# Kernel optimization log

Measured on AMD Instinct MI355X. Metric: run time of the kernel, lower is better.

The kernel has to match this reference:

```python
import jax, jax.numpy as jnp
import numpy as np
from jax import lax

C = 64
B, H, W = 4, 192, 192


def conv2d(x, w, b):
    # x: [B,C,H,W], w: [O,I,3,3] (OIHW), stride 1, pad 1
    y = lax.conv_general_dilated(x, w, (1, 1), ((1, 1), (1, 1)),
                                 dimension_numbers=("NCHW", "OIHW", "NCHW"))
    return y + b[None, :, None, None]


def csm(x, w1, b1, w2, b2):
    # residual block: conv3x3 -> relu -> conv3x3 + skip
    return x + conv2d(jax.nn.relu(conv2d(x, w1, b1)), w2, b2)


def setup_inputs() -> dict:
    key = jax.random.key(0)
    ks = jax.random.split(key, 12)
    s = 1.0 / np.sqrt(C * 9)
    def cw(k):
        return jax.random.uniform(k, (C, C, 3, 3), jnp.float32, -s, s)
    def cb(k):
        return jax.random.uniform(k, (C,), jnp.float32, -s, s)
    return {
        "low1": jax.random.normal(ks[0], (B, C, H, W), jnp.float32),
        "low2": jax.random.normal(ks[1], (B, C, H, W), jnp.float32),
        "fe1_w1": cw(ks[2]), "fe1_b1": cb(ks[3]),
        "fe1_w2": cw(ks[4]), "fe1_b2": cb(ks[5]),
        "fe2_w1": cw(ks[6]), "fe2_b1": cb(ks[7]),
        "fe2_w2": cw(ks[8]), "fe2_b2": cb(ks[9]),
        "conv_w": cw(ks[10]), "conv_b": cb(ks[11]),
    }


def reference(low1, low2, fe1_w1, fe1_b1, fe1_w2, fe1_b2,
              fe2_w1, fe2_b1, fe2_w2, fe2_b2, conv_w, conv_b):
    Q1 = conv2d(csm(low1, fe1_w1, fe1_b1, fe1_w2, fe1_b2), conv_w, conv_b)
    K1 = conv2d(csm(low2, fe1_w1, fe1_b1, fe1_w2, fe1_b2), conv_w, conv_b)
    Q2 = conv2d(csm(low1, fe2_w1, fe2_b1, fe2_w2, fe2_b2), conv_w, conv_b)
    K2 = conv2d(csm(low2, fe2_w1, fe2_b1, fe2_w2, fe2_b2), conv_w, conv_b)

    # per-row cross-width scores: [B,H,W,W] (no scaling; softmax then relu)
    score1 = jax.nn.relu(jax.nn.softmax(jnp.einsum("bchw,bchv->bhwv", Q1, K1), axis=-1))
    score2 = jax.nn.relu(jax.nn.softmax(jnp.einsum("bchw,bchv->bhwv", Q2, K2), axis=-1))

    def apply_score(score, feat):
        # out[b,c,h,w] = sum_v score[b,h,w,v] * feat[b,c,h,v]
        return jnp.einsum("bhwv,bchv->bchw", score, feat)

    def apply_score_T(score, feat):
        # out[b,c,h,w] = sum_v score[b,h,v,w] * feat[b,c,h,v]
        return jnp.einsum("bhvw,bchv->bchw", score, feat)

    right2left1 = apply_score(score1, low2)
    right2left2 = apply_score(score2, low2)
    left2right1 = apply_score_T(score1, low1)
    left2right2 = apply_score_T(score2, low1)
    left2right2left = apply_score(score2, left2right1)
    right2left2right = apply_score_T(score2, right2left1)

    left = low1 + right2left1 + right2left2 + left2right2left
    right = low2 + left2right1 + left2right2 + right2left2right
    return (left, right)
```

## Files before the change

kernel.cpp:

```cpp
#include <hip/hip_runtime.h>
#include <stdint.h>

#define NB 4
#define NC 64
#define NH 192
#define NW 192

typedef __attribute__((ext_vector_type(8))) short bf16x8;
typedef __attribute__((ext_vector_type(4))) float f32x4;
typedef unsigned short u16;
typedef unsigned int u32;

__device__ inline float bf2f(u16 x){ u32 u = ((u32)x) << 16; return __builtin_bit_cast(float, u); }
__device__ inline u16 f2bf(float f){ u32 u = __builtin_bit_cast(u32, f); u32 r = u + 0x7fffu + ((u >> 16) & 1u); return (u16)(r >> 16); }
__device__ inline bf16x8 packf8(float4 a, float4 b){
  bf16x8 r;
  r[0]=(short)f2bf(a.x); r[1]=(short)f2bf(a.y); r[2]=(short)f2bf(a.z); r[3]=(short)f2bf(a.w);
  r[4]=(short)f2bf(b.x); r[5]=(short)f2bf(b.y); r[6]=(short)f2bf(b.z); r[7]=(short)f2bf(b.w);
  return r;
}

__global__ void wxform_k(const float* __restrict__ w0, const float* __restrict__ w1,
                         const float* __restrict__ w2, const float* __restrict__ w3,
                         const float* __restrict__ w4, u16* __restrict__ out){
  int idx = blockIdx.x * 256 + threadIdx.x;
  if (idx >= 5 * 36864) return;
  int t = idx / 36864, e = idx % 36864;
  int r = e >> 12, rem = e & 4095, co = rem >> 6, ci = rem & 63;
  const float* src = (t == 0) ? w0 : (t == 1) ? w1 : (t == 2) ? w2 : (t == 3) ? w3 : w4;
  out[idx] = f2bf(src[co * 576 + ci * 9 + r]);
}

__global__ __launch_bounds__(192) void nchw2nhwc_k(const float* __restrict__ in, u16* __restrict__ out){
  int bh = blockIdx.x; int b = bh / NH, h = bh % NH;
  int w = threadIdx.x;
  u16 v[64];
  const float* p = in + ((size_t)b * NC * NH + h) * NW + w;
#pragma unroll
  for (int c = 0; c < 64; ++c) v[c] = f2bf(p[(size_t)c * NH * NW]);
  uint4* q4 = (uint4*)(out + ((size_t)bh * NW + w) * NC);
#pragma unroll
  for (int i = 0; i < 8; ++i){
    uint4 t;
    t.x = (u32)v[i*8+0] | ((u32)v[i*8+1] << 16);
    t.y = (u32)v[i*8+2] | ((u32)v[i*8+3] << 16);
    t.z = (u32)v[i*8+4] | ((u32)v[i*8+5] << 16);
    t.w = (u32)v[i*8+6] | ((u32)v[i*8+7] << 16);
    q4[i] = t;
  }
}

__global__ __launch_bounds__(256) void bf2f_k(const u16* __restrict__ in, float* __restrict__ out){
  int i = blockIdx.x * 256 + threadIdx.x;
  uint4 v = ((const uint4*)in)[i];
  float4 f0, f1;
  f0.x = bf2f((u16)(v.x & 0xffff)); f0.y = bf2f((u16)(v.x >> 16));
  f0.z = bf2f((u16)(v.y & 0xffff)); f0.w = bf2f((u16)(v.y >> 16));
  f1.x = bf2f((u16)(v.z & 0xffff)); f1.y = bf2f((u16)(v.z >> 16));
  f1.z = bf2f((u16)(v.w & 0xffff)); f1.w = bf2f((u16)(v.w >> 16));
  ((float4*)out)[2*i]   = f0;
  ((float4*)out)[2*i+1] = f1;
}

__global__ __launch_bounds__(256) void conv3_k(const u16* __restrict__ in, const u16* __restrict__ wt,
    const float* __restrict__ bias, const u16* __restrict__ skip, u16* __restrict__ out, int relu){
  __shared__ __align__(16) u16 xr[3][98 * 72];
  int blk = blockIdx.x;
  int wh = blk & 1;
  int strip = blk >> 1;
  int g0 = strip * 3;
  int b = g0 / NH, h0 = g0 % NH;
  int wstart = wh * 96;
  int tid = threadIdx.x;
  int wvv = tid >> 6, lane = tid & 63, l15 = lane & 15, qd = lane >> 4;
  int mh = wvv >> 1, wq = wvv & 1;

#define STAGE(hh_) do { \
    int hh = (hh_); \
    int slot = ((hh % 3) + 3) % 3; \
    bool rowok = (hh >= 0) && (hh < NH); \
    const u16* src = in + (((size_t)b * NH + (rowok ? hh : 0)) * NW) * 64; \
    for (int k2 = tid; k2 < 784; k2 += 256){ \
      int x = k2 >> 3, part = k2 & 7; \
      int w = wstart - 1 + x; \
      uint4 val = make_uint4(0,0,0,0); \
      if (rowok && w >= 0 && w < NW) val = *(const uint4*)(src + (size_t)w * 64 + part * 8); \
      *(uint4*)&xr[slot][x * 72 + part * 8] = val; \
    } \
  } while(0)

  STAGE(h0 - 1);
  STAGE(h0);
  for (int j = 0; j < 3; ++j){
    int h = h0 + j;
    STAGE(h + 1);
    __syncthreads();
    f32x4 acc[2][3];
#pragma unroll
    for (int mt = 0; mt < 2; ++mt)
#pragma unroll
      for (int nt = 0; nt < 3; ++nt) acc[mt][nt] = (f32x4){0.f,0.f,0.f,0.f};
#pragma unroll
    for (int r = 0; r < 9; ++r){
      int ky = r / 3, kx = r % 3;
      int hs = h - 1 + ky;
      const u16* xbase = xr[((hs % 3) + 3) % 3];
#pragma unroll
      for (int ks = 0; ks < 2; ++ks){
        int ci = ks * 32 + qd * 8;
        const u16* wp = wt + r * 4096 + ci;
        bf16x8 a0 = *(const bf16x8*)(wp + (mh * 32 + l15) * 64);
        bf16x8 a1 = *(const bf16x8*)(wp + (mh * 32 + 16 + l15) * 64);
#pragma unroll
        for (int nt = 0; nt < 3; ++nt){
          int x = wq * 48 + nt * 16 + l15 + kx;
          bf16x8 bfr = *(const bf16x8*)&xr[0][0 + ((hs % 3) + 3) % 3 * 0];
          bfr = *(const bf16x8*)&xbase[x * 72 + ci];
          acc[0][nt] = __builtin_amdgcn_mfma_f32_16x16x32_bf16(a0, bfr, acc[0][nt], 0, 0, 0);
          acc[1][nt] = __builtin_amdgcn_mfma_f32_16x16x32_bf16(a1, bfr, acc[1][nt], 0, 0, 0);
        }
      }
    }
    size_t rowbase = ((size_t)(b * NH + h)) * NW * 64;
#pragma unroll
    for (int mt = 0; mt < 2; ++mt){
      int co0 = mh * 32 + mt * 16 + qd * 4;
      float4 bb = *(const float4*)(bias + co0);
#pragma unroll
      for (int nt = 0; nt < 3; ++nt){
        int w = wstart + wq * 48 + nt * 16 + l15;
        size_t o = rowbase + (size_t)w * 64 + co0;
        float v0 = acc[mt][nt][0] + bb.x, v1 = acc[mt][nt][1] + bb.y;
        float v2 = acc[mt][nt][2] + bb.z, v3 = acc[mt][nt][3] + bb.w;
        if (relu){ v0 = fmaxf(v0,0.f); v1 = fmaxf(v1,0.f); v2 = fmaxf(v2,0.f); v3 = fmaxf(v3,0.f); }
        if (skip){
          uint2 ss = *(const uint2*)(skip + o);
          v0 += bf2f((u16)(ss.x & 0xffff)); v1 += bf2f((u16)(ss.x >> 16));
          v2 += bf2f((u16)(ss.y & 0xffff)); v3 += bf2f((u16)(ss.y >> 16));
        }
        uint2 st;
        st.x = (u32)f2bf(v0) | ((u32)f2bf(v1) << 16);
        st.y = (u32)f2bf(v2) | ((u32)f2bf(v3) << 16);
        *(uint2*)(out + o) = st;
      }
    }
    __syncthreads();
  }
#undef STAGE
}

template<int XYF32>
__global__ __launch_bounds__(256) void attn_k(const u16* __restrict__ Q, const u16* __restrict__ K,
    const void* __restrict__ Xv, const void* __restrict__ Yv,
    u16* __restrict__ outA, u16* __restrict__ outB){
  __shared__ __align__(16) u16 P [192 * 200];
  __shared__ __align__(16) u16 Pt[192 * 200];
  int bh = blockIdx.x, b = bh / NH, h = bh % NH;
  int tid = threadIdx.x, wv = tid >> 6, lane = tid & 63, l15 = lane & 15, qd = lane >> 4;
  size_t rowo = (size_t)bh * NW * 64;
  const u16* Qr = Q + rowo; const u16* Kr = K + rowo;
  const size_t CS = (size_t)NH * NW;
  size_t xb0 = (size_t)b * 64 * CS + (size_t)h * NW;
  const float* Xf = (const float*)Xv; const float* Yf = (const float*)Yv;
  const u16* Xb = (const u16*)Xv; const u16* Yb = (const u16*)Yv;

#pragma unroll 1
  for (int mi = 0; mi < 3; ++mi){
    int mt = wv * 3 + mi;
    f32x4 s[12];
#pragma unroll
    for (int nt = 0; nt < 12; ++nt) s[nt] = (f32x4){0,0,0,0};
#pragma unroll
    for (int ks = 0; ks < 2; ++ks){
      bf16x8 aq = *(const bf16x8*)(Qr + (mt * 16 + l15) * 64 + ks * 32 + qd * 8);
#pragma unroll
      for (int nt = 0; nt < 12; ++nt){
        bf16x8 bk = *(const bf16x8*)(Kr + (nt * 16 + l15) * 64 + ks * 32 + qd * 8);
        s[nt] = __builtin_amdgcn_mfma_f32_16x16x32_bf16(aq, bk, s[nt], 0, 0, 0);
      }
    }
#pragma unroll
    for (int rg = 0; rg < 4; ++rg){
      float mx = -1e30f;
#pragma unroll
      for (int nt = 0; nt < 12; ++nt) mx = fmaxf(mx, s[nt][rg]);
      mx = fmaxf(mx, __shfl_xor(mx, 1));
      mx = fmaxf(mx, __shfl_xor(mx, 2));
      mx = fmaxf(mx, __shfl_xor(mx, 4));
      mx = fmaxf(mx, __shfl_xor(mx, 8));
      float sum = 0.f;
#pragma unroll
      for (int nt = 0; nt < 12; ++nt){ float ev = __expf(s[nt][rg] - mx); s[nt][rg] = ev; sum += ev; }
      sum += __shfl_xor(sum, 1);
      sum += __shfl_xor(sum, 2);
      sum += __shfl_xor(sum, 4);
      sum += __shfl_xor(sum, 8);
      float inv = 1.f / sum;
      int w = mt * 16 + qd * 4 + rg;
#pragma unroll
      for (int nt = 0; nt < 12; ++nt){
        float val = s[nt][rg] * inv;
        s[nt][rg] = val;
        P[w * 200 + nt * 16 + l15] = f2bf(val);
      }
    }
#pragma unroll
    for (int nt = 0; nt < 12; ++nt){
      uint2 pk;
      pk.x = (u32)f2bf(s[nt][0]) | ((u32)f2bf(s[nt][1]) << 16);
      pk.y = (u32)f2bf(s[nt][2]) | ((u32)f2bf(s[nt][3]) << 16);
      *(uint2*)&Pt[(nt * 16 + l15) * 200 + mt * 16 + qd * 4] = pk;
    }
  }
  __syncthreads();

  f32x4 accA[3][4], accB[3][4];
#pragma unroll
  for (int ni = 0; ni < 3; ++ni)
#pragma unroll
    for (int mt = 0; mt < 4; ++mt){ accA[ni][mt] = (f32x4){0,0,0,0}; accB[ni][mt] = (f32x4){0,0,0,0}; }
#pragma unroll 1
  for (int ks = 0; ks < 6; ++ks){
    int v0 = ks * 32 + qd * 8;
    bf16x8 aX[4], aY[4];
#pragma unroll
    for (int mt = 0; mt < 4; ++mt){
      int c = mt * 16 + l15;
      size_t off = xb0 + (size_t)c * CS + v0;
      if (XYF32){
        float4 x0 = *(const float4*)(Xf + off), x1 = *(const float4*)(Xf + off + 4);
        float4 y0 = *(const float4*)(Yf + off), y1 = *(const float4*)(Yf + off + 4);
        aX[mt] = packf8(x0, x1); aY[mt] = packf8(y0, y1);
      } else {
        aX[mt] = *(const bf16x8*)(Xb + off);
        aY[mt] = *(const bf16x8*)(Yb + off);
      }
    }
#pragma unroll
    for (int ni = 0; ni < 3; ++ni){
      int wrow = (wv * 3 + ni) * 16 + l15;
      bf16x8 bP  = *(const bf16x8*)&P [wrow * 200 + v0];
      bf16x8 bPt = *(const bf16x8*)&Pt[wrow * 200 + v0];
#pragma unroll
      for (int mt = 0; mt < 4; ++mt){
        accA[ni][mt] = __builtin_amdgcn_mfma_f32_16x16x32_bf16(aX[mt], bP,  accA[ni][mt], 0, 0, 0);
        accB[ni][mt] = __builtin_amdgcn_mfma_f32_16x16x32_bf16(aY[mt], bPt, accB[ni][mt], 0, 0, 0);
      }
    }
  }
#pragma unroll
  for (int ni = 0; ni < 3; ++ni){
    int w = (wv * 3 + ni) * 16 + l15;
#pragma unroll
    for (int mt = 0; mt < 4; ++mt){
#pragma unroll
      for (int rg = 0; rg < 4; ++rg){
        int c = mt * 16 + qd * 4 + rg;
        size_t o = xb0 + (size_t)c * CS + w;
        float ra = XYF32 ? Yf[o] : bf2f(Yb[o]);
        float rb = XYF32 ? Xf[o] : bf2f(Xb[o]);
        outA[o] = f2bf(accA[ni][mt][rg] + ra);
        outB[o] = f2bf(accB[ni][mt][rg] + rb);
      }
    }
  }
}

extern "C" void kernel_launch(void* const* d_in, const int* in_sizes, int n_in,
                              void* d_out, int out_size, void* d_ws, size_t ws_size,
                              hipStream_t stream){
  const float* low1 = (const float*)d_in[0];
  const float* low2 = (const float*)d_in[1];
  const float* b11 = (const float*)d_in[3];
  const float* b12 = (const float*)d_in[5];
  const float* b21 = (const float*)d_in[7];
  const float* b22 = (const float*)d_in[9];
  const float* bcv = (const float*)d_in[11];
  const size_t BUF = (size_t)NB * NH * NW * NC;
  u16* WT = (u16*)d_ws;
  u16* s1 = WT + 184320;
  u16* s2 = s1 + BUF;
  u16* o1 = (u16*)d_out;
  u16* o2 = o1 + BUF;
  u16* o3 = o1 + 2 * BUF;
  u16* o4 = o1 + 3 * BUF;
  float* outL = (float*)d_out;
  float* outR = outL + BUF;

  wxform_k<<<dim3(720), dim3(256), 0, stream>>>(
      (const float*)d_in[2], (const float*)d_in[4], (const float*)d_in[6],
      (const float*)d_in[8], (const float*)d_in[10], WT);
  nchw2nhwc_k<<<dim3(NB * NH), dim3(192), 0, stream>>>(low1, o1);
  nchw2nhwc_k<<<dim3(NB * NH), dim3(192), 0, stream>>>(low2, o2);

#define CONV(in_, wti, bias_, skip_, out_, relu_) \
  conv3_k<<<dim3(512), dim3(256), 0, stream>>>(in_, WT + (wti) * 36864, bias_, skip_, out_, relu_)

  CONV(o1, 0, b11, (const u16*)nullptr, o3, 1);
  CONV(o3, 1, b12, o1, o4, 0);
  CONV(o4, 4, bcv, (const u16*)nullptr, s1, 0);
  CONV(o2, 0, b11, (const u16*)nullptr, o3, 1);
  CONV(o3, 1, b12, o2, o4, 0);
  CONV(o4, 4, bcv, (const u16*)nullptr, s2, 0);
  attn_k<1><<<dim3(NB * NH), dim3(256), 0, stream>>>(s1, s2, (const void*)low2, (const void*)low1, o3, o4);
  CONV(o1, 2, b21, (const u16*)nullptr, s1, 1);
  CONV(s1, 3, b22, o1, s2, 0);
  CONV(s2, 4, bcv, (const u16*)nullptr, o1, 0);
  CONV(o2, 2, b21, (const u16*)nullptr, s1, 1);
  CONV(s1, 3, b22, o2, s2, 0);
  CONV(s2, 4, bcv, (const u16*)nullptr, o2, 0);
  attn_k<0><<<dim3(NB * NH), dim3(256), 0, stream>>>(o1, o2, (const void*)o4, (const void*)o3, s1, s2);
  bf2f_k<<<dim3((int)(BUF / 8 / 256)), dim3(256), 0, stream>>>(s1, outL);
  bf2f_k<<<dim3((int)(BUF / 8 / 256)), dim3(256), 0, stream>>>(s2, outR);
#undef CONV
}
```

Measured before the change: 639.3 us.

## Batch paired convs per launch, shrink conv tiles, drop attention transpose buffer

Each conv launch now handles both input streams at once, with 64-wide width chunks, giving 1536 blocks with launch bounds of 4 instead of 512 blocks per tensor; this cuts the number of launches and raises occupancy. The attention kernel drops its separate transposed-probability LDS buffer and runs the two apply passes one after another, building the transposed operand with strided 16-bit gathers from the single buffer. The final attention writes the left output directly in fp32, which removes one bf16-to-fp32 conversion kernel, and buffers are reused so the residual-conv output can be written in place. The risks are less weight reuse in the smaller conv tiles and bank-conflicted scalar LDS gathers in the transposed pass.

```diff
diff --git a/kernel.cpp b/kernel.cpp
--- a/kernel.cpp
+++ b/kernel.cpp
@@ -62,27 +62,32 @@
   ((float4*)out)[2*i+1] = f1;
 }
 
-__global__ __launch_bounds__(256) void conv3_k(const u16* __restrict__ in, const u16* __restrict__ wt,
-    const float* __restrict__ bias, const u16* __restrict__ skip, u16* __restrict__ out, int relu){
-  __shared__ __align__(16) u16 xr[3][98 * 72];
+__global__ __launch_bounds__(256, 4) void conv3_k(
+    const u16* __restrict__ in1, const u16* __restrict__ in2,
+    const u16* __restrict__ wt, const float* __restrict__ bias,
+    const u16* __restrict__ skip1, const u16* __restrict__ skip2,
+    u16* __restrict__ out1, u16* __restrict__ out2, int relu){
+  __shared__ __align__(16) u16 xr[3][66 * 72];
   int blk = blockIdx.x;
-  int wh = blk & 1;
-  int strip = blk >> 1;
-  int g0 = strip * 3;
-  int b = g0 / NH, h0 = g0 % NH;
-  int wstart = wh * 96;
+  int inp = blk & 1, rest = blk >> 1;
+  int chunk = rest % 3, strip = rest / 3;
+  const u16* in = inp ? in2 : in1;
+  const u16* skip = inp ? skip2 : skip1;
+  u16* out = inp ? out2 : out1;
+  int g0 = strip * 3, b = g0 / NH, h0 = g0 % NH;
+  int w0c = chunk * 64;
   int tid = threadIdx.x;
   int wvv = tid >> 6, lane = tid & 63, l15 = lane & 15, qd = lane >> 4;
   int mh = wvv >> 1, wq = wvv & 1;
 
 #define STAGE(hh_) do { \
     int hh = (hh_); \
-    int slot = ((hh % 3) + 3) % 3; \
+    int slot = (hh + 3) % 3; \
     bool rowok = (hh >= 0) && (hh < NH); \
-    const u16* src = in + (((size_t)b * NH + (rowok ? hh : 0)) * NW) * 64; \
-    for (int k2 = tid; k2 < 784; k2 += 256){ \
+    const u16* src = in + ((size_t)(b * NH + (rowok ? hh : 0)) * NW) * 64; \
+    for (int k2 = tid; k2 < 528; k2 += 256){ \
       int x = k2 >> 3, part = k2 & 7; \
-      int w = wstart - 1 + x; \
+      int w = w0c - 1 + x; \
       uint4 val = make_uint4(0,0,0,0); \
       if (rowok && w >= 0 && w < NW) val = *(const uint4*)(src + (size_t)w * 64 + part * 8); \
       *(uint4*)&xr[slot][x * 72 + part * 8] = val; \
@@ -95,16 +100,16 @@
     int h = h0 + j;
     STAGE(h + 1);
     __syncthreads();
-    f32x4 acc[2][3];
+    f32x4 acc[2][2];
 #pragma unroll
     for (int mt = 0; mt < 2; ++mt)
 #pragma unroll
-      for (int nt = 0; nt < 3; ++nt) acc[mt][nt] = (f32x4){0.f,0.f,0.f,0.f};
+      for (int nt = 0; nt < 2; ++nt) acc[mt][nt] = (f32x4){0.f,0.f,0.f,0.f};
 #pragma unroll
     for (int r = 0; r < 9; ++r){
       int ky = r / 3, kx = r % 3;
       int hs = h - 1 + ky;
-      const u16* xbase = xr[((hs % 3) + 3) % 3];
+      const u16* xb = xr[(hs + 3) % 3];
 #pragma unroll
       for (int ks = 0; ks < 2; ++ks){
         int ci = ks * 32 + qd * 8;
@@ -112,10 +117,9 @@
         bf16x8 a0 = *(const bf16x8*)(wp + (mh * 32 + l15) * 64);
         bf16x8 a1 = *(const bf16x8*)(wp + (mh * 32 + 16 + l15) * 64);
 #pragma unroll
-        for (int nt = 0; nt < 3; ++nt){
-          int x = wq * 48 + nt * 16 + l15 + kx;
-          bf16x8 bfr = *(const bf16x8*)&xr[0][0 + ((hs % 3) + 3) % 3 * 0];
-          bfr = *(const bf16x8*)&xbase[x * 72 + ci];
+        for (int nt = 0; nt < 2; ++nt){
+          int x = wq * 32 + nt * 16 + l15 + kx;
+          bf16x8 bfr = *(const bf16x8*)&xb[x * 72 + ci];
           acc[0][nt] = __builtin_amdgcn_mfma_f32_16x16x32_bf16(a0, bfr, acc[0][nt], 0, 0, 0);
           acc[1][nt] = __builtin_amdgcn_mfma_f32_16x16x32_bf16(a1, bfr, acc[1][nt], 0, 0, 0);
         }
@@ -127,8 +131,8 @@
       int co0 = mh * 32 + mt * 16 + qd * 4;
       float4 bb = *(const float4*)(bias + co0);
 #pragma unroll
-      for (int nt = 0; nt < 3; ++nt){
-        int w = wstart + wq * 48 + nt * 16 + l15;
+      for (int nt = 0; nt < 2; ++nt){
+        int w = w0c + wq * 32 + nt * 16 + l15;
         size_t o = rowbase + (size_t)w * 64 + co0;
         float v0 = acc[mt][nt][0] + bb.x, v1 = acc[mt][nt][1] + bb.y;
         float v2 = acc[mt][nt][2] + bb.z, v3 = acc[mt][nt][3] + bb.w;
@@ -149,12 +153,11 @@
 #undef STAGE
 }
 
-template<int XYF32>
-__global__ __launch_bounds__(256) void attn_k(const u16* __restrict__ Q, const u16* __restrict__ K,
+template<int XYF32, int AF32>
+__global__ __launch_bounds__(256, 2) void attn_k(const u16* __restrict__ Q, const u16* __restrict__ K,
     const void* __restrict__ Xv, const void* __restrict__ Yv,
-    u16* __restrict__ outA, u16* __restrict__ outB){
-  __shared__ __align__(16) u16 P [192 * 200];
-  __shared__ __align__(16) u16 Pt[192 * 200];
+    void* __restrict__ outAv, u16* __restrict__ outB){
+  __shared__ __align__(16) u16 P[192 * 200];
   int bh = blockIdx.x, b = bh / NH, h = bh % NH;
   int tid = threadIdx.x, wv = tid >> 6, lane = tid & 63, l15 = lane & 15, qd = lane >> 4;
   size_t rowo = (size_t)bh * NW * 64;
@@ -198,70 +201,97 @@
       float inv = 1.f / sum;
       int w = mt * 16 + qd * 4 + rg;
 #pragma unroll
-      for (int nt = 0; nt < 12; ++nt){
-        float val = s[nt][rg] * inv;
-        s[nt][rg] = val;
-        P[w * 200 + nt * 16 + l15] = f2bf(val);
-      }
-    }
-#pragma unroll
-    for (int nt = 0; nt < 12; ++nt){
-      uint2 pk;
-      pk.x = (u32)f2bf(s[nt][0]) | ((u32)f2bf(s[nt][1]) << 16);
-      pk.y = (u32)f2bf(s[nt][2]) | ((u32)f2bf(s[nt][3]) << 16);
-      *(uint2*)&Pt[(nt * 16 + l15) * 200 + mt * 16 + qd * 4] = pk;
+      for (int nt = 0; nt < 12; ++nt)
+        P[w * 200 + nt * 16 + l15] = f2bf(s[nt][rg] * inv);
     }
   }
   __syncthreads();
 
-  f32x4 accA[3][4], accB[3][4];
-#pragma unroll
-  for (int ni = 0; ni < 3; ++ni)
-#pragma unroll
-    for (int mt = 0; mt < 4; ++mt){ accA[ni][mt] = (f32x4){0,0,0,0}; accB[ni][mt] = (f32x4){0,0,0,0}; }
+  {
+    f32x4 acc[3][4];
+#pragma unroll
+    for (int ni = 0; ni < 3; ++ni)
+#pragma unroll
+      for (int mt = 0; mt < 4; ++mt) acc[ni][mt] = (f32x4){0,0,0,0};
 #pragma unroll 1
-  for (int ks = 0; ks < 6; ++ks){
-    int v0 = ks * 32 + qd * 8;
-    bf16x8 aX[4], aY[4];
-#pragma unroll
-    for (int mt = 0; mt < 4; ++mt){
-      int c = mt * 16 + l15;
-      size_t off = xb0 + (size_t)c * CS + v0;
-      if (XYF32){
-        float4 x0 = *(const float4*)(Xf + off), x1 = *(const float4*)(Xf + off + 4);
-        float4 y0 = *(const float4*)(Yf + off), y1 = *(const float4*)(Yf + off + 4);
-        aX[mt] = packf8(x0, x1); aY[mt] = packf8(y0, y1);
-      } else {
-        aX[mt] = *(const bf16x8*)(Xb + off);
-        aY[mt] = *(const bf16x8*)(Yb + off);
+    for (int ks = 0; ks < 6; ++ks){
+      int v0 = ks * 32 + qd * 8;
+      bf16x8 a[4];
+#pragma unroll
+      for (int mt = 0; mt < 4; ++mt){
+        size_t off = xb0 + (size_t)(mt * 16 + l15) * CS + v0;
+        if (XYF32){
+          float4 x0 = *(const float4*)(Xf + off), x1 = *(const float4*)(Xf + off + 4);
+          a[mt] = packf8(x0, x1);
+        } else a[mt] = *(const bf16x8*)(Xb + off);
+      }
+#pragma unroll
+      for (int ni = 0; ni < 3; ++ni){
+        int wrow = (wv * 3 + ni) * 16 + l15;
+        bf16x8 bP = *(const bf16x8*)&P[wrow * 200 + v0];
+#pragma unroll
+        for (int mt = 0; mt < 4; ++mt)
+          acc[ni][mt] = __builtin_amdgcn_mfma_f32_16x16x32_bf16(a[mt], bP, acc[ni][mt], 0, 0, 0);
       }
     }
 #pragma unroll
     for (int ni = 0; ni < 3; ++ni){
-      int wrow = (wv * 3 + ni) * 16 + l15;
-      bf16x8 bP  = *(const bf16x8*)&P [wrow * 200 + v0];
-      bf16x8 bPt = *(const bf16x8*)&Pt[wrow * 200 + v0];
+      int w = (wv * 3 + ni) * 16 + l15;
+#pragma unroll
+      for (int mt = 0; mt < 4; ++mt)
+#pragma unroll
+        for (int rg = 0; rg < 4; ++rg){
+          int c = mt * 16 + qd * 4 + rg;
+          size_t o = xb0 + (size_t)c * CS + w;
+          float ra = XYF32 ? Yf[o] : bf2f(Yb[o]);
+          float val = acc[ni][mt][rg] + ra;
+          if (AF32) ((float*)outAv)[o] = val;
+          else ((u16*)outAv)[o] = f2bf(val);
+        }
+    }
+  }
+  __syncthreads();
+  {
+    f32x4 acc[3][4];
+#pragma unroll
+    for (int ni = 0; ni < 3; ++ni)
+#pragma unroll
+      for (int mt = 0; mt < 4; ++mt) acc[ni][mt] = (f32x4){0,0,0,0};
+#pragma unroll 1
+    for (int ks = 0; ks < 6; ++ks){
+      int v0 = ks * 32 + qd * 8;
+      bf16x8 a[4];
 #pragma unroll
       for (int mt = 0; mt < 4; ++mt){
-        accA[ni][mt] = __builtin_amdgcn_mfma_f32_16x16x32_bf16(aX[mt], bP,  accA[ni][mt], 0, 0, 0);
-        accB[ni][mt] = __builtin_amdgcn_mfma_f32_16x16x32_bf16(aY[mt], bPt, accB[ni][mt], 0, 0, 0);
-      }
-    }
-  }
-#pragma unroll
-  for (int ni = 0; ni < 3; ++ni){
-    int w = (wv * 3 + ni) * 16 + l15;
-#pragma unroll
-    for (int mt = 0; mt < 4; ++mt){
-#pragma unroll
-      for (int rg = 0; rg < 4; ++rg){
-        int c = mt * 16 + qd * 4 + rg;
-        size_t o = xb0 + (size_t)c * CS + w;
-        float ra = XYF32 ? Yf[o] : bf2f(Yb[o]);
-        float rb = XYF32 ? Xf[o] : bf2f(Xb[o]);
-        outA[o] = f2bf(accA[ni][mt][rg] + ra);
-        outB[o] = f2bf(accB[ni][mt][rg] + rb);
-      }
+        size_t off = xb0 + (size_t)(mt * 16 + l15) * CS + v0;
+        if (XYF32){
+          float4 y0 = *(const float4*)(Yf + off), y1 = *(const float4*)(Yf + off + 4);
+          a[mt] = packf8(y0, y1);
+        } else a[mt] = *(const bf16x8*)(Yb + off);
+      }
+#pragma unroll
+      for (int ni = 0; ni < 3; ++ni){
+        int wrow = (wv * 3 + ni) * 16 + l15;
+        bf16x8 bPt;
+#pragma unroll
+        for (int jj = 0; jj < 8; ++jj) bPt[jj] = (short)P[(v0 + jj) * 200 + wrow];
+#pragma unroll
+        for (int mt = 0; mt < 4; ++mt)
+          acc[ni][mt] = __builtin_amdgcn_mfma_f32_16x16x32_bf16(a[mt], bPt, acc[ni][mt], 0, 0, 0);
+      }
+    }
+#pragma unroll
+    for (int ni = 0; ni < 3; ++ni){
+      int w = (wv * 3 + ni) * 16 + l15;
+#pragma unroll
+      for (int mt = 0; mt < 4; ++mt)
+#pragma unroll
+        for (int rg = 0; rg < 4; ++rg){
+          int c = mt * 16 + qd * 4 + rg;
+          size_t o = xb0 + (size_t)c * CS + w;
+          float rb = XYF32 ? Xf[o] : bf2f(Xb[o]);
+          outB[o] = f2bf(acc[ni][mt][rg] + rb);
+        }
     }
   }
 }
@@ -293,24 +323,19 @@
   nchw2nhwc_k<<<dim3(NB * NH), dim3(192), 0, stream>>>(low1, o1);
   nchw2nhwc_k<<<dim3(NB * NH), dim3(192), 0, stream>>>(low2, o2);
 
-#define CONV(in_, wti, bias_, skip_, out_, relu_) \
-  conv3_k<<<dim3(512), dim3(256), 0, stream>>>(in_, WT + (wti) * 36864, bias_, skip_, out_, relu_)
-
-  CONV(o1, 0, b11, (const u16*)nullptr, o3, 1);
-  CONV(o3, 1, b12, o1, o4, 0);
-  CONV(o4, 4, bcv, (const u16*)nullptr, s1, 0);
-  CONV(o2, 0, b11, (const u16*)nullptr, o3, 1);
-  CONV(o3, 1, b12, o2, o4, 0);
-  CONV(o4, 4, bcv, (const u16*)nullptr, s2, 0);
-  attn_k<1><<<dim3(NB * NH), dim3(256), 0, stream>>>(s1, s2, (const void*)low2, (const void*)low1, o3, o4);
-  CONV(o1, 2, b21, (const u16*)nullptr, s1, 1);
-  CONV(s1, 3, b22, o1, s2, 0);
-  CONV(s2, 4, bcv, (const u16*)nullptr, o1, 0);
-  CONV(o2, 2, b21, (const u16*)nullptr, s1, 1);
-  CONV(s1, 3, b22, o2, s2, 0);
-  CONV(s2, 4, bcv, (const u16*)nullptr, o2, 0);
-  attn_k<0><<<dim3(NB * NH), dim3(256), 0, stream>>>(o1, o2, (const void*)o4, (const void*)o3, s1, s2);
-  bf2f_k<<<dim3((int)(BUF / 8 / 256)), dim3(256), 0, stream>>>(s1, outL);
+#define CONVP(iA, iB, wti, bias_, sA, sB, oA, oB, relu_) \
+  conv3_k<<<dim3(1536), dim3(256), 0, stream>>>(iA, iB, WT + (wti) * 36864, bias_, sA, sB, oA, oB, relu_)
+
+  CONVP(o1, o2, 0, b11, (const u16*)nullptr, (const u16*)nullptr, o3, o4, 1);
+  CONVP(o3, o4, 1, b12, o1, o2, s1, s2, 0);
+  CONVP(s1, s2, 4, bcv, (const u16*)nullptr, (const u16*)nullptr, o3, o4, 0);
+  attn_k<1, 0><<<dim3(NB * NH), dim3(256), 0, stream>>>(
+      o3, o4, (const void*)low2, (const void*)low1, (void*)s1, s2);
+  CONVP(o1, o2, 2, b21, (const u16*)nullptr, (const u16*)nullptr, o3, o4, 1);
+  CONVP(o3, o4, 3, b22, o1, o2, o1, o2, 0);
+  CONVP(o1, o2, 4, bcv, (const u16*)nullptr, (const u16*)nullptr, o3, o4, 0);
+  attn_k<0, 1><<<dim3(NB * NH), dim3(256), 0, stream>>>(
+      o3, o4, (const void*)s2, (const void*)s1, (void*)outL, s2);
   bf2f_k<<<dim3((int)(BUF / 8 / 256)), dim3(256), 0, stream>>>(s2, outR);
-#undef CONV
-}
+#undef CONVP
+}
```

Result: slower. 901.8 us (+41.1%).
